# Kernel tuning notes

Measured on AMD Instinct MI355X. Metric: run time of the kernel, lower is better.

Reference implementation:

```python
import jax, jax.numpy as jnp
import numpy as np
from jax import lax

N, D, K, R, T = 200000, 128, 64, 4, 50000
L = 2 * R  # positive + negative relation layers
ITERATIONS = 2


def _l2norm(x, eps=1e-12):
    # torch F.normalize(p=2): x / max(||x||, eps)
    n = jnp.sqrt(jnp.sum(x * x, axis=-1, keepdims=True))
    return x / jnp.maximum(n, eps)


def setup_inputs() -> dict:
    key = jax.random.key(0)
    ks = jax.random.split(key, 8)
    # Unique write targets (a permutation) so the last-write scatter is deterministic;
    # matches input_specs' randint intent (indices uniform in [0, N)).
    perm = jax.random.permutation(ks[0], N)
    subj_idx = perm[:T].astype(jnp.int32)
    obj_idx = perm[T:2 * T].astype(jnp.int32)
    layer_idx = jax.random.randint(ks[1], (T,), 0, L, dtype=jnp.int32)
    memberships = jax.random.randint(ks[2], (N, K), 0, 2, dtype=jnp.int32)
    embedding_m = jax.random.normal(ks[3], (N, D), dtype=jnp.float32)
    # ClassUpdate params: [d+K] -> d
    Wc = jax.random.normal(ks[4], (D + K, D), dtype=jnp.float32) / np.sqrt(D + K)
    bc = jnp.zeros((D,), dtype=jnp.float32)
    # RelationUpdate params, one layer per (relation, polarity): [2d] -> [2d]
    Wr = jax.random.normal(ks[5], (L, 2 * D, 2 * D), dtype=jnp.float32) / np.sqrt(2 * D)
    br = jnp.zeros((L, 2 * D), dtype=jnp.float32)
    return {
        'embedding_m': embedding_m,
        'memberships': memberships,
        'subj_idx': subj_idx,
        'obj_idx': obj_idx,
        'layer_idx': layer_idx,
        'Wc': Wc, 'bc': bc, 'Wr': Wr, 'br': br,
    }


def reference(embedding_m, memberships, subj_idx, obj_idx, layer_idx, Wc, bc, Wr, br):
    mem = memberships.astype(embedding_m.dtype)  # [N, K]
    t_ar = jnp.arange(T)

    def iteration(e, _):
        # --- ClassUpdate: e' = l2norm(tanh([e; m] Wc + bc)) ---
        x = jnp.concatenate([e, mem], axis=1)           # [N, d+K]
        e = _l2norm(jnp.tanh(x @ Wc + bc))              # [N, d]
        # --- RelationUpdates: reads come from the post-class-update snapshot `e`
        pair = jnp.concatenate([e[subj_idx], e[obj_idx]], axis=1)   # [T, 2d]
        # compute through all L relation layers, then select each triple's layer
        out_all = jnp.einsum('tc,lcd->tld', pair, Wr) + br          # [T, L, 2d]
        out = jnp.tanh(out_all[t_ar, layer_idx])                    # [T, 2d]
        new_s = _l2norm(out[:, :D])
        new_o = _l2norm(out[:, D:])
        e_next = e.at[subj_idx].set(new_s).at[obj_idx].set(new_o)
        return e_next, None

    e_final, _ = lax.scan(iteration, embedding_m, None, length=ITERATIONS)
    return e_final
```

## Files before the change

kernel.cpp:

```cpp
#include <hip/hip_runtime.h>
#include <hip/hip_bf16.h>


#define NROWS 200000
#define DD    128
#define KK    64
#define TT    50000
#define LL    8
#define BT    64
#define PADT  50560
#define NPASS 3125

#define NB    100
#define CHB   500
#define PL    8
#define PREPB 268
#define MBB   6250

#define WS_OFFS   0
#define WS_CNT    64
#define WS_BASE   4096
#define WS_BINS   8192
#define WS_WCP    210432
#define WS_WRP    (WS_WCP + 6*8*64*16)
#define WS_MB     (WS_WRP + 8*8*16*64*16)
#define WS_E16    (WS_MB + NROWS*8)
#define WS_NEED   (WS_E16 + (size_t)NROWS*DD*2)

typedef unsigned short u16;
typedef unsigned int   u32;
typedef unsigned long long u64;
typedef unsigned char  u8;
typedef __attribute__((ext_vector_type(8))) short bf16x8;
typedef __attribute__((ext_vector_type(4))) float f32x4;
typedef __attribute__((ext_vector_type(4))) unsigned int u32x4;

#define SWZ(row, byte) ((byte) ^ (((row)&7)<<4))

__device__ __forceinline__ u32 bfbits(float f){
  __hip_bfloat16 h = __float2bfloat16(f);
  return (u32)*reinterpret_cast<unsigned short*>(&h);
}
__device__ __forceinline__ u32 pk(float lo, float hi){
  return bfbits(lo) | (bfbits(hi) << 16);
}
__device__ __forceinline__ float qreduce16(float ss){
  ss += __shfl_xor(ss, 1, 64);
  ss += __shfl_xor(ss, 2, 64);
  ss += __shfl_xor(ss, 4, 64);
  ss += __shfl_xor(ss, 8, 64);
  return ss;
}
__device__ __forceinline__ float fast_tanh(float x){
  float a = fabsf(x);
  float e = __expf(-2.0f*a);
  float t = (1.0f - e) * __builtin_amdgcn_rcpf(1.0f + e);
  return copysignf(t, x);
}
__device__ __forceinline__ float rnorm_scale(float ss){
  return __builtin_amdgcn_rcpf(fmaxf(__builtin_amdgcn_sqrtf(ss), 1e-12f));
}
__device__ __forceinline__ void nt_store_v4(void* p, u32x4 v){
  __builtin_nontemporal_store(v, (u32x4*)p);
}

__global__ __launch_bounds__(256) void k_prep(
    const float* __restrict__ Wc, const float* __restrict__ Wr,
    uint4* __restrict__ wcp, uint4* __restrict__ wrp,
    const int* __restrict__ layer, int* __restrict__ cnt,
    const int* __restrict__ mem, u8* __restrict__ mb8)
{
  if (blockIdx.x >= PREPB + NB){
    int gid = (blockIdx.x - PREPB - NB)*256 + threadIdx.x;
    const int4* s4 = (const int4*)(mem + (size_t)gid*8);
    int4 a = s4[0], b = s4[1];
    u8 byte = (u8)((a.x!=0) | ((a.y!=0)<<1) | ((a.z!=0)<<2) | ((a.w!=0)<<3)
             | ((b.x!=0)<<4) | ((b.y!=0)<<5) | ((b.z!=0)<<6) | ((b.w!=0)<<7));
    __builtin_nontemporal_store(byte, &mb8[gid]);
    return;
  }
  if (blockIdx.x >= PREPB){
    const int bb = blockIdx.x - PREPB, lane = threadIdx.x;
    if (lane >= 64) return;
    const int lim = bb*CHB + CHB;
    int i0 = bb*CHB + lane*PL, i1 = i0 + PL; if (i1 > lim) i1 = lim;
    int c[LL] = {0,0,0,0,0,0,0,0};
    for (int i = i0; i < i1; ++i){
      int l = layer[i];
      #pragma unroll
      for (int k = 0; k < LL; ++k) c[k] += (l == k);
    }
    #pragma unroll
    for (int k = 0; k < LL; ++k){
      int v = c[k];
      v += __shfl_xor(v, 1, 64); v += __shfl_xor(v, 2, 64);
      v += __shfl_xor(v, 4, 64); v += __shfl_xor(v, 8, 64);
      v += __shfl_xor(v, 16, 64); v += __shfl_xor(v, 32, 64);
      if (lane == k) cnt[bb*LL + k] = v;
    }
    return;
  }
  int id = blockIdx.x*blockDim.x + threadIdx.x;
  if (id < 3072){
    int lane = id & 63, nt = (id >> 6) & 7, kt = id >> 9;
    int k0 = kt*32 + (lane>>4)*8, n = nt*16 + (lane&15);
    u32 p[4];
    #pragma unroll
    for (int e2 = 0; e2 < 4; ++e2)
      p[e2] = pk(Wc[(k0 + 2*e2)*DD + n], Wc[(k0 + 2*e2 + 1)*DD + n]);
    wcp[id] = make_uint4(p[0], p[1], p[2], p[3]);
  } else if (id < 3072 + 65536){
    int id2 = id - 3072;
    int lane = id2 & 63, nt = (id2>>6) & 15, kt = (id2>>10) & 7, l = id2 >> 13;
    int k0 = kt*32 + (lane>>4)*8, n = nt*16 + (lane&15);
    const float* w = Wr + (size_t)l*65536;
    u32 p[4];
    #pragma unroll
    for (int e2 = 0; e2 < 4; ++e2)
      p[e2] = pk(w[(k0 + 2*e2)*256 + n], w[(k0 + 2*e2 + 1)*256 + n]);
    wrp[id2] = make_uint4(p[0], p[1], p[2], p[3]);
  }
}

__global__ __launch_bounds__(64) void k_bin2(const int* __restrict__ cnt,
                                             int* __restrict__ offs,
                                             int* __restrict__ gbase,
                                             int* __restrict__ bins)
{
  __shared__ int pre[NB][LL];
  __shared__ int tot[LL], soffs[LL+1];
  const int t = threadIdx.x;
  if (t < LL){
    int acc = 0;
    for (int bb = 0; bb < NB; ++bb){ pre[bb][t] = acc; acc += cnt[bb*LL + t]; }
    tot[t] = acc;
  }
  __syncthreads();
  if (t == 0){
    int acc = 0;
    for (int l = 0; l < LL; ++l){
      soffs[l] = acc; offs[l] = acc;
      acc += ((tot[l] + BT - 1)/BT)*BT;
    }
    soffs[LL] = acc; offs[LL] = acc;
  }
  __syncthreads();
  for (int idx = t; idx < NB*LL; idx += 64){
    int bb = idx >> 3, k = idx & 7;
    gbase[idx] = soffs[k] + pre[bb][k];
  }
  const int k = t >> 3, sub = t & 7;
  const int sz = soffs[k+1] - soffs[k];
  for (int i = tot[k] + sub; i < sz; i += 8) bins[soffs[k] + i] = -1;
}

__global__ __launch_bounds__(64) void k_bin3(const int* __restrict__ layer,
                                             const int* __restrict__ gbase,
                                             int* __restrict__ bins)
{
  const int bb = blockIdx.x, lane = threadIdx.x;
  const int lim = bb*CHB + CHB;
  int i0 = bb*CHB + lane*PL, i1 = i0 + PL; if (i1 > lim) i1 = lim;
  int c[LL] = {0,0,0,0,0,0,0,0};
  for (int i = i0; i < i1; ++i){
    int l = layer[i];
    #pragma unroll
    for (int k = 0; k < LL; ++k) c[k] += (l == k);
  }
  int start[LL];
  #pragma unroll
  for (int k = 0; k < LL; ++k){
    int v = c[k];
    #pragma unroll
    for (int d = 1; d < 64; d <<= 1){
      int u = __shfl_up(v, d, 64);
      if (lane >= d) v += u;
    }
    start[k] = gbase[bb*LL + k] + v - c[k];
  }
  for (int i = i0; i < i1; ++i){
    int l = layer[i];
    #pragma unroll
    for (int k = 0; k < LL; ++k)
      if (l == k) bins[start[k]++] = i;
  }
}

template<bool S16, bool W16, bool WF32>
__global__ __launch_bounds__(256) void k_class(
    const float* __restrict__ srcf, const u16* __restrict__ src16,
    u16* __restrict__ e16, float* __restrict__ dstf,
    const u64* __restrict__ mbits,
    const uint4* __restrict__ wcp, const float* __restrict__ bc)
{
  __shared__ __align__(16) char smem[32768];
  __shared__ float sPart[64][4];
  u16* sA = (u16*)smem;

  const int tid = threadIdx.x;
  const int lane = tid & 63, wid = tid >> 6;
  const int colj = lane & 15, qw = lane >> 4;
  const int rowbase = blockIdx.x * 64;

  int erow[4], ecol[4];
  uint4  eA[4];
  float4 fA[4][2];
  #pragma unroll
  for (int v = 0; v < 4; ++v){
    int f = (v*256 + tid) * 8;
    erow[v] = f >> 7; ecol[v] = f & 127;
    if constexpr (S16){
      eA[v] = *(const uint4*)(src16 + (size_t)(rowbase+erow[v])*DD + ecol[v]);
    } else {
      const float4* s4 = (const float4*)(srcf + (size_t)(rowbase+erow[v])*DD + ecol[v]);
      fA[v][0] = s4[0]; fA[v][1] = s4[1];
    }
  }
  const u64 mv = mbits[rowbase + (tid >> 2)];

  bf16x8 wf[6][2];
  #pragma unroll
  for (int kt = 0; kt < 6; ++kt)
    #pragma unroll
    for (int j = 0; j < 2; ++j)
      wf[kt][j] = *(const bf16x8*)&wcp[(kt*8 + 2*wid + j)*64 + lane];
  const float b0 = bc[(2*wid)*16 + colj];
  const float b1 = bc[(2*wid+1)*16 + colj];

  #pragma unroll
  for (int v = 0; v < 4; ++v){
    uint4 out;
    if constexpr (S16){
      out = eA[v];
    } else {
      float4 a = fA[v][0], b = fA[v][1];
      out = make_uint4(pk(a.x,a.y), pk(a.z,a.w), pk(b.x,b.y), pk(b.z,b.w));
    }
    *(uint4*)((char*)sA + erow[v]*384 + SWZ(erow[v], ecol[v]*2)) = out;
  }
  {
    const int r = tid >> 2, q = tid & 3;
    u32 s = (u32)(mv >> (q*16)) & 0xFFFFu;
    u32 p[8];
    #pragma unroll
    for (int jj = 0; jj < 8; ++jj){
      u32 lo = (s >> (2*jj))     & 1u;
      u32 hi = (s >> (2*jj + 1)) & 1u;
      p[jj] = (lo ? 0x3F80u : 0u) | (hi ? 0x3F800000u : 0u);
    }
    *(uint4*)((char*)sA + r*384 + SWZ(r, 256 + q*32))      = make_uint4(p[0],p[1],p[2],p[3]);
    *(uint4*)((char*)sA + r*384 + SWZ(r, 256 + q*32 + 16)) = make_uint4(p[4],p[5],p[6],p[7]);
  }
  __syncthreads();

  f32x4 acc[4][2];
  #pragma unroll
  for (int m = 0; m < 4; ++m){
    acc[m][0] = (f32x4){0.f,0.f,0.f,0.f};
    acc[m][1] = (f32x4){0.f,0.f,0.f,0.f};
  }
  #pragma unroll
  for (int m = 0; m < 4; ++m){
    int row = m*16 + colj;
    #pragma unroll
    for (int kt = 0; kt < 6; ++kt){
      bf16x8 afr = *(bf16x8*)((char*)sA + row*384 + SWZ(row, kt*64 + qw*16));
      acc[m][0] = __builtin_amdgcn_mfma_f32_16x16x32_bf16(afr, wf[kt][0], acc[m][0], 0,0,0);
      acc[m][1] = __builtin_amdgcn_mfma_f32_16x16x32_bf16(afr, wf[kt][1], acc[m][1], 0,0,0);
    }
  }
  #pragma unroll
  for (int m = 0; m < 4; ++m){
    #pragma unroll
    for (int r = 0; r < 4; ++r){
      float t0 = fast_tanh(acc[m][0][r] + b0);
      float t1 = fast_tanh(acc[m][1][r] + b1);
      acc[m][0][r] = t0; acc[m][1][r] = t1;
      float ss = qreduce16(t0*t0 + t1*t1);
      if (colj == 0) sPart[m*16 + qw*4 + r][wid] = ss;
    }
  }
  __syncthreads();

  #pragma unroll
  for (int m = 0; m < 4; ++m){
    #pragma unroll
    for (int r = 0; r < 4; ++r){
      int tri = m*16 + qw*4 + r;
      f32x4 p = *(f32x4*)sPart[tri];
      float sc = rnorm_scale(p[0] + p[1] + p[2] + p[3]);
      float v0 = acc[m][0][r]*sc, v1 = acc[m][1][r]*sc;
      int c0 = wid*32 + colj;
      if constexpr (W16){
        u16* so = (u16*)smem;
        so[tri*128 + c0]      = (u16)bfbits(v0);
        so[tri*128 + c0 + 16] = (u16)bfbits(v1);
      }
      if constexpr (WF32){
        float* so = (float*)smem;
        so[tri*128 + c0]      = v0;
        so[tri*128 + c0 + 16] = v1;
      }
    }
  }
  __syncthreads();

  if constexpr (W16){
    const u32x4* sp = (const u32x4*)smem;
    u32x4* gp = (u32x4*)(e16 + (size_t)rowbase*DD);
    #pragma unroll
    for (int k = 0; k < 4; ++k)
      nt_store_v4(gp + tid + k*256, sp[tid + k*256]);
  }
  if constexpr (WF32){
    const u32x4* sp = (const u32x4*)smem;
    u32x4* gp = (u32x4*)(dstf + (size_t)rowbase*DD);
    #pragma unroll
    for (int k = 0; k < 8; ++k)
      nt_store_v4(gp + tid + k*256, sp[tid + k*256]);
  }
}

template<bool S16, bool W16, bool WF32>
__global__ __launch_bounds__(256) void k_rel(
    const float* __restrict__ ef32, u16* __restrict__ e16,
    float* __restrict__ dstf,
    const int* __restrict__ subj, const int* __restrict__ obj,
    const uint4* __restrict__ wrp, const float* __restrict__ br,
    const int* __restrict__ offs, const int* __restrict__ bins)
{
  __shared__ __align__(16) char smem[32768];
  __shared__ float sBr[256];
  __shared__ float sPart[BT][4];
  __shared__ int   sS[BT], sO[BT];
  u16* sA = (u16*)smem;

  const int tid  = threadIdx.x;
  const int base = blockIdx.x * BT;
  if (base >= offs[LL]) return;
  int l = 0;
  while (l < LL-1 && base >= offs[l+1]) ++l;

  const int lane = tid & 63, wid = tid >> 6;
  const int colj = lane & 15, qw = lane >> 4;

  const uint4* wb = wrp + (size_t)l*8192 + lane;
  bf16x8 wf[8][4];
  #pragma unroll
  for (int n = 0; n < 4; ++n){
    wf[0][n] = *(const bf16x8*)&wb[(0*16 + wid*4 + n)*64];
    wf[1][n] = *(const bf16x8*)&wb[(1*16 + wid*4 + n)*64];
  }

  sBr[tid] = br[l*256 + tid];

  const int ti = tid >> 2, q = tid & 3;
  int id = bins[base + ti];
  int rs = -1, ro = -1;
  if (id >= 0){ rs = subj[id]; ro = obj[id]; }
  if (q == 0){ sS[ti] = rs; sO[ti] = ro; }
  const int rr = (q < 2) ? rs : ro;
  if constexpr (S16){
    const u16* srcp = e16 + (size_t)rr*DD + (q & 1)*64;
    #pragma unroll
    for (int j = 0; j < 8; ++j){
      uint4 w = (id >= 0) ? ((const uint4*)srcp)[j] : make_uint4(0u,0u,0u,0u);
      *(uint4*)((char*)sA + ti*512 + SWZ(ti, q*128 + j*16)) = w;
    }
  } else {
    const float* srcp = ef32 + (size_t)rr*DD + (q & 1)*64;
    #pragma unroll
    for (int j = 0; j < 8; ++j){
      uint4 w;
      if (id >= 0){
        float4 a = ((const float4*)srcp)[2*j], b = ((const float4*)srcp)[2*j+1];
        w = make_uint4(pk(a.x,a.y), pk(a.z,a.w), pk(b.x,b.y), pk(b.z,b.w));
      } else w = make_uint4(0u,0u,0u,0u);
      *(uint4*)((char*)sA + ti*512 + SWZ(ti, q*128 + j*16)) = w;
    }
  }
  __syncthreads();

  f32x4 acc[4][4];
  #pragma unroll
  for (int m = 0; m < 4; ++m)
    #pragma unroll
    for (int n = 0; n < 4; ++n) acc[m][n] = (f32x4){0.f,0.f,0.f,0.f};

  #pragma unroll
  for (int kt = 0; kt < 8; ++kt){
    if (kt + 2 < 8){
      #pragma unroll
      for (int n = 0; n < 4; ++n)
        wf[kt+2][n] = *(const bf16x8*)&wb[((kt+2)*16 + wid*4 + n)*64];
    }
    #pragma unroll
    for (int m = 0; m < 4; ++m){
      int row = m*16 + colj;
      bf16x8 afr = *(bf16x8*)((char*)sA + row*512 + SWZ(row, kt*64 + qw*16));
      #pragma unroll
      for (int n = 0; n < 4; ++n)
        acc[m][n] = __builtin_amdgcn_mfma_f32_16x16x32_bf16(afr, wf[kt][n], acc[m][n], 0,0,0);
    }
  }

  #pragma unroll
  for (int m = 0; m < 4; ++m){
    #pragma unroll
    for (int n = 0; n < 4; ++n){
      float b = sBr[(wid*4 + n)*16 + colj];
      #pragma unroll
      for (int r = 0; r < 4; ++r)
        acc[m][n][r] = fast_tanh(acc[m][n][r] + b);
    }
    #pragma unroll
    for (int r = 0; r < 4; ++r){
      float ss = acc[m][0][r]*acc[m][0][r] + acc[m][1][r]*acc[m][1][r]
               + acc[m][2][r]*acc[m][2][r] + acc[m][3][r]*acc[m][3][r];
      ss = qreduce16(ss);
      if (colj == 0) sPart[m*16 + qw*4 + r][wid] = ss;
    }
  }
  __syncthreads();

  const int h = wid >> 1;
  if constexpr (W16){
    #pragma unroll
    for (int m = 0; m < 4; ++m){
      #pragma unroll
      for (int r = 0; r < 4; ++r){
        int tri = m*16 + qw*4 + r;
        float ss = sPart[tri][2*h] + sPart[tri][2*h + 1];
        float sc = rnorm_scale(ss);
        #pragma unroll
        for (int n = 0; n < 4; ++n){
          int col = (wid*4 + n)*16 + colj;
          float v = acc[m][n][r]*sc;
          *(u16*)((char*)smem + tri*512 + ((col*2) ^ ((tri&7)<<4))) = (u16)bfbits(v);
        }
      }
    }
    __syncthreads();
    #pragma unroll
    for (int k = 0; k < 8; ++k){
      int c = tid + k*256;
      int tri = c >> 5, hh = (c >> 4) & 1, sub = c & 15;
      int row = hh ? sO[tri] : sS[tri];
      if (row >= 0){
        u32x4 v = *(const u32x4*)((char*)smem + ((c*16) ^ ((tri&7)<<4)));
        nt_store_v4((u32x4*)(e16 + (size_t)row*DD) + sub, v);
      }
    }
  }
  if constexpr (WF32){
    #pragma unroll
    for (int m = 0; m < 4; ++m){
      #pragma unroll
      for (int r = 0; r < 4; ++r){
        int tri = m*16 + qw*4 + r;
        int row = h ? sO[tri] : sS[tri];
        if (row < 0) continue;
        float ss = sPart[tri][2*h] + sPart[tri][2*h + 1];
        float sc = rnorm_scale(ss);
        #pragma unroll
        for (int n = 0; n < 4; ++n){
          int cc = (wid*4 + n)*16 + colj - h*DD;
          __builtin_nontemporal_store(acc[m][n][r]*sc, &dstf[(size_t)row*DD + cc]);
        }
      }
    }
  }
}

extern "C" void kernel_launch(void* const* d_in, const int* in_sizes, int n_in,
                              void* d_out, int out_size, void* d_ws, size_t ws_size,
                              hipStream_t stream) {
  (void)in_sizes; (void)n_in; (void)out_size;
  const float* emb  = (const float*)d_in[0];
  const int*   mem  = (const int*)  d_in[1];
  const int*   subj = (const int*)  d_in[2];
  const int*   obj  = (const int*)  d_in[3];
  const int*   lay  = (const int*)  d_in[4];
  const float* Wc   = (const float*)d_in[5];
  const float* bc   = (const float*)d_in[6];
  const float* Wr   = (const float*)d_in[7];
  const float* br   = (const float*)d_in[8];

  float* e   = (float*)d_out;
  char*  wsb = (char*)d_ws;
  int*   offs  = (int*)(wsb + WS_OFFS);
  int*   cnt   = (int*)(wsb + WS_CNT);
  int*   gbase = (int*)(wsb + WS_BASE);
  int*   bins  = (int*)(wsb + WS_BINS);
  uint4* wcp   = (uint4*)(wsb + WS_WCP);
  uint4* wrp   = (uint4*)(wsb + WS_WRP);
  u64*   mbits = (u64*)(wsb + WS_MB);
  u8*    mb8   = (u8*)(wsb + WS_MB);
  u16*   e16   = (u16*)(wsb + WS_E16);

  k_prep<<<PREPB + NB + MBB, 256, 0, stream>>>(Wc, Wr, wcp, wrp, lay, cnt, mem, mb8);
  k_bin2<<<1, 64, 0, stream>>>(cnt, offs, gbase, bins);
  k_bin3<<<NB, 64, 0, stream>>>(lay, gbase, bins);

  if (ws_size >= WS_NEED){
    k_class<false,true,false><<<NPASS, 256, 0, stream>>>(
        emb, nullptr, e16, nullptr, mbits, wcp, bc);
    k_rel<true,true,false><<<PADT/BT, 256, 0, stream>>>(
        nullptr, e16, nullptr, subj, obj, wrp, br, offs, bins);
    k_class<true,false,true><<<NPASS, 256, 0, stream>>>(
        nullptr, e16, nullptr, e, mbits, wcp, bc);
    k_rel<false,false,true><<<PADT/BT, 256, 0, stream>>>(
        e, nullptr, e, subj, obj, wrp, br, offs, bins);
  } else {
    k_class<false,false,true><<<NPASS, 256, 0, stream>>>(
        emb, nullptr, nullptr, e, mbits, wcp, bc);
    k_rel<false,false,true><<<PADT/BT, 256, 0, stream>>>(
        e, nullptr, e, subj, obj, wrp, br, offs, bins);
    k_class<false,false,true><<<NPASS, 256, 0, stream>>>(
        e, nullptr, nullptr, e, mbits, wcp, bc);
    k_rel<false,false,true><<<PADT/BT, 256, 0, stream>>>(
        e, nullptr, e, subj, obj, wrp, br, offs, bins);
  }
}
```

Baseline: 172.0 us.

## Split class-update work across 8 waves and write fp32 output directly

After: 174.6 us. About the same (+1.5%).

```diff
diff --git a/kernel.cpp b/kernel.cpp
--- a/kernel.cpp
+++ b/kernel.cpp
@@ -187,14 +187,15 @@
 }
 
 template<bool S16, bool W16, bool WF32>
-__global__ __launch_bounds__(256) void k_class(
+__global__ __launch_bounds__(512) void k_class(
     const float* __restrict__ srcf, const u16* __restrict__ src16,
     u16* __restrict__ e16, float* __restrict__ dstf,
     const u64* __restrict__ mbits,
     const uint4* __restrict__ wcp, const float* __restrict__ bc)
 {
-  __shared__ __align__(16) char smem[32768];
-  __shared__ float sPart[64][4];
+  __shared__ __align__(16) char smem[24576];
+  __shared__ float sPart[64][9];
+  __shared__ float sScale[64];
   u16* sA = (u16*)smem;
 
   const int tid = threadIdx.x;
@@ -202,43 +203,41 @@
   const int colj = lane & 15, qw = lane >> 4;
   const int rowbase = blockIdx.x * 64;
 
-  int erow[4], ecol[4];
-  uint4  eA[4];
-  float4 fA[4][2];
-  #pragma unroll
-  for (int v = 0; v < 4; ++v){
-    int f = (v*256 + tid) * 8;
-    erow[v] = f >> 7; ecol[v] = f & 127;
+  int crow[2], ccc[2];
+  uint4  eA[2];
+  float4 fA[2][2];
+  #pragma unroll
+  for (int v = 0; v < 2; ++v){
+    int c = tid + v*512;
+    crow[v] = c >> 4; ccc[v] = c & 15;
     if constexpr (S16){
-      eA[v] = *(const uint4*)(src16 + (size_t)(rowbase+erow[v])*DD + ecol[v]);
+      eA[v] = *(const uint4*)(src16 + (size_t)(rowbase+crow[v])*DD + ccc[v]*8);
     } else {
-      const float4* s4 = (const float4*)(srcf + (size_t)(rowbase+erow[v])*DD + ecol[v]);
+      const float4* s4 = (const float4*)(srcf + (size_t)(rowbase+crow[v])*DD + ccc[v]*8);
       fA[v][0] = s4[0]; fA[v][1] = s4[1];
     }
   }
-  const u64 mv = mbits[rowbase + (tid >> 2)];
-
-  bf16x8 wf[6][2];
+  u64 mv = 0;
+  if (tid < 256) mv = mbits[rowbase + (tid >> 2)];
+
+  bf16x8 wf[6];
   #pragma unroll
   for (int kt = 0; kt < 6; ++kt)
-    #pragma unroll
-    for (int j = 0; j < 2; ++j)
-      wf[kt][j] = *(const bf16x8*)&wcp[(kt*8 + 2*wid + j)*64 + lane];
-  const float b0 = bc[(2*wid)*16 + colj];
-  const float b1 = bc[(2*wid+1)*16 + colj];
-
-  #pragma unroll
-  for (int v = 0; v < 4; ++v){
+    wf[kt] = *(const bf16x8*)&wcp[(kt*8 + wid)*64 + lane];
+  const float b = bc[wid*16 + colj];
+
+  #pragma unroll
+  for (int v = 0; v < 2; ++v){
     uint4 out;
     if constexpr (S16){
       out = eA[v];
     } else {
-      float4 a = fA[v][0], b = fA[v][1];
-      out = make_uint4(pk(a.x,a.y), pk(a.z,a.w), pk(b.x,b.y), pk(b.z,b.w));
-    }
-    *(uint4*)((char*)sA + erow[v]*384 + SWZ(erow[v], ecol[v]*2)) = out;
-  }
-  {
+      float4 a = fA[v][0], bb2 = fA[v][1];
+      out = make_uint4(pk(a.x,a.y), pk(a.z,a.w), pk(bb2.x,bb2.y), pk(bb2.z,bb2.w));
+    }
+    *(uint4*)((char*)sA + crow[v]*384 + SWZ(crow[v], ccc[v]*16)) = out;
+  }
+  if (tid < 256){
     const int r = tid >> 2, q = tid & 3;
     u32 s = (u32)(mv >> (q*16)) & 0xFFFFu;
     u32 p[8];
@@ -253,71 +252,62 @@
   }
   __syncthreads();
 
-  f32x4 acc[4][2];
-  #pragma unroll
-  for (int m = 0; m < 4; ++m){
-    acc[m][0] = (f32x4){0.f,0.f,0.f,0.f};
-    acc[m][1] = (f32x4){0.f,0.f,0.f,0.f};
-  }
+  f32x4 acc[4];
+  #pragma unroll
+  for (int m = 0; m < 4; ++m) acc[m] = (f32x4){0.f,0.f,0.f,0.f};
   #pragma unroll
   for (int m = 0; m < 4; ++m){
     int row = m*16 + colj;
     #pragma unroll
     for (int kt = 0; kt < 6; ++kt){
       bf16x8 afr = *(bf16x8*)((char*)sA + row*384 + SWZ(row, kt*64 + qw*16));
-      acc[m][0] = __builtin_amdgcn_mfma_f32_16x16x32_bf16(afr, wf[kt][0], acc[m][0], 0,0,0);
-      acc[m][1] = __builtin_amdgcn_mfma_f32_16x16x32_bf16(afr, wf[kt][1], acc[m][1], 0,0,0);
+      acc[m] = __builtin_amdgcn_mfma_f32_16x16x32_bf16(afr, wf[kt], acc[m], 0,0,0);
     }
   }
   #pragma unroll
   for (int m = 0; m < 4; ++m){
     #pragma unroll
     for (int r = 0; r < 4; ++r){
-      float t0 = fast_tanh(acc[m][0][r] + b0);
-      float t1 = fast_tanh(acc[m][1][r] + b1);
-      acc[m][0][r] = t0; acc[m][1][r] = t1;
-      float ss = qreduce16(t0*t0 + t1*t1);
+      float t = fast_tanh(acc[m][r] + b);
+      acc[m][r] = t;
+      float ss = qreduce16(t*t);
       if (colj == 0) sPart[m*16 + qw*4 + r][wid] = ss;
     }
   }
   __syncthreads();
-
-  #pragma unroll
-  for (int m = 0; m < 4; ++m){
-    #pragma unroll
-    for (int r = 0; r < 4; ++r){
-      int tri = m*16 + qw*4 + r;
-      f32x4 p = *(f32x4*)sPart[tri];
-      float sc = rnorm_scale(p[0] + p[1] + p[2] + p[3]);
-      float v0 = acc[m][0][r]*sc, v1 = acc[m][1][r]*sc;
-      int c0 = wid*32 + colj;
-      if constexpr (W16){
-        u16* so = (u16*)smem;
-        so[tri*128 + c0]      = (u16)bfbits(v0);
-        so[tri*128 + c0 + 16] = (u16)bfbits(v1);
+  if (tid < 64){
+    float s = 0.f;
+    #pragma unroll
+    for (int i = 0; i < 8; ++i) s += sPart[tid][i];
+    sScale[tid] = rnorm_scale(s);
+  }
+  __syncthreads();
+
+  if constexpr (W16){
+    u16* so = (u16*)smem;
+    #pragma unroll
+    for (int m = 0; m < 4; ++m){
+      #pragma unroll
+      for (int r = 0; r < 4; ++r){
+        int row = m*16 + qw*4 + r;
+        so[row*128 + wid*16 + colj] = (u16)bfbits(acc[m][r]*sScale[row]);
       }
-      if constexpr (WF32){
-        float* so = (float*)smem;
-        so[tri*128 + c0]      = v0;
-        so[tri*128 + c0 + 16] = v1;
-      }
-    }
-  }
-  __syncthreads();
-
-  if constexpr (W16){
+    }
+    __syncthreads();
     const u32x4* sp = (const u32x4*)smem;
     u32x4* gp = (u32x4*)(e16 + (size_t)rowbase*DD);
-    #pragma unroll
-    for (int k = 0; k < 4; ++k)
-      nt_store_v4(gp + tid + k*256, sp[tid + k*256]);
+    nt_store_v4(gp + tid,       sp[tid]);
+    nt_store_v4(gp + tid + 512, sp[tid + 512]);
   }
   if constexpr (WF32){
-    const u32x4* sp = (const u32x4*)smem;
-    u32x4* gp = (u32x4*)(dstf + (size_t)rowbase*DD);
-    #pragma unroll
-    for (int k = 0; k < 8; ++k)
-      nt_store_v4(gp + tid + k*256, sp[tid + k*256]);
+    #pragma unroll
+    for (int m = 0; m < 4; ++m){
+      #pragma unroll
+      for (int r = 0; r < 4; ++r){
+        int row = m*16 + qw*4 + r;
+        dstf[(size_t)(rowbase+row)*DD + wid*16 + colj] = acc[m][r]*sScale[row];
+      }
+    }
   }
 }
 
@@ -465,7 +455,7 @@
         #pragma unroll
         for (int n = 0; n < 4; ++n){
           int cc = (wid*4 + n)*16 + colj - h*DD;
-          __builtin_nontemporal_store(acc[m][n][r]*sc, &dstf[(size_t)row*DD + cc]);
+          dstf[(size_t)row*DD + cc] = acc[m][n][r]*sc;
         }
       }
     }
@@ -503,20 +493,20 @@
   k_bin3<<<NB, 64, 0, stream>>>(lay, gbase, bins);
 
   if (ws_size >= WS_NEED){
-    k_class<false,true,false><<<NPASS, 256, 0, stream>>>(
+    k_class<false,true,false><<<NPASS, 512, 0, stream>>>(
         emb, nullptr, e16, nullptr, mbits, wcp, bc);
     k_rel<true,true,false><<<PADT/BT, 256, 0, stream>>>(
         nullptr, e16, nullptr, subj, obj, wrp, br, offs, bins);
-    k_class<true,false,true><<<NPASS, 256, 0, stream>>>(
+    k_class<true,false,true><<<NPASS, 512, 0, stream>>>(
         nullptr, e16, nullptr, e, mbits, wcp, bc);
     k_rel<false,false,true><<<PADT/BT, 256, 0, stream>>>(
         e, nullptr, e, subj, obj, wrp, br, offs, bins);
   } else {
-    k_class<false,false,true><<<NPASS, 256, 0, stream>>>(
+    k_class<false,false,true><<<NPASS, 512, 0, stream>>>(
         emb, nullptr, nullptr, e, mbits, wcp, bc);
     k_rel<false,false,true><<<PADT/BT, 256, 0, stream>>>(
         e, nullptr, e, subj, obj, wrp, br, offs, bins);
-    k_class<false,false,true><<<NPASS, 256, 0, stream>>>(
+    k_class<false,false,true><<<NPASS, 512, 0, stream>>>(
         e, nullptr, nullptr, e, mbits, wcp, bc);
     k_rel<false,false,true><<<PADT/BT, 256, 0, stream>>>(
         e, nullptr, e, subj, obj, wrp, br, offs, bins);
```

## Fuse class and relation phases into one persistent cooperative kernel with grid syncs

Applied to the files above, without the earlier changes.

Result: slower. 437.6 us (+154.4%).

```diff
diff --git a/kernel.cpp b/kernel.cpp
--- a/kernel.cpp
+++ b/kernel.cpp
@@ -1,5 +1,8 @@
 #include <hip/hip_runtime.h>
 #include <hip/hip_bf16.h>
+#include <hip/hip_cooperative_groups.h>
+
+namespace cg = cooperative_groups;
 
 
 #define NROWS 200000
@@ -9,6 +12,7 @@
 #define LL    8
 #define BT    64
 #define PADT  50560
+#define NGRP  (PADT/BT)
 #define NPASS 3125
 
 #define NB    100
@@ -27,6 +31,13 @@
 #define WS_E16    (WS_MB + NROWS*8)
 #define WS_NEED   (WS_E16 + (size_t)NROWS*DD*2)
 
+#define SM_BYTES  35328
+#define SM_SA     0
+#define SM_BR     32768
+#define SM_PART   33792
+#define SM_SS     34816
+#define SM_SO     35072
+
 typedef unsigned short u16;
 typedef unsigned int   u32;
 typedef unsigned long long u64;
@@ -186,37 +197,19 @@
   }
 }
 
-template<bool S16, bool W16, bool WF32>
-__global__ __launch_bounds__(256) void k_class(
+template<bool S16, bool W16>
+__device__ void class_phase(char* smem,
     const float* __restrict__ srcf, const u16* __restrict__ src16,
-    u16* __restrict__ e16, float* __restrict__ dstf,
+    u16* __restrict__ e16o, float* __restrict__ dstf,
     const u64* __restrict__ mbits,
     const uint4* __restrict__ wcp, const float* __restrict__ bc)
 {
-  __shared__ __align__(16) char smem[32768];
-  __shared__ float sPart[64][4];
   u16* sA = (u16*)smem;
+  float (*sPart)[4] = (float(*)[4])(smem + SM_PART);
 
   const int tid = threadIdx.x;
   const int lane = tid & 63, wid = tid >> 6;
   const int colj = lane & 15, qw = lane >> 4;
-  const int rowbase = blockIdx.x * 64;
-
-  int erow[4], ecol[4];
-  uint4  eA[4];
-  float4 fA[4][2];
-  #pragma unroll
-  for (int v = 0; v < 4; ++v){
-    int f = (v*256 + tid) * 8;
-    erow[v] = f >> 7; ecol[v] = f & 127;
-    if constexpr (S16){
-      eA[v] = *(const uint4*)(src16 + (size_t)(rowbase+erow[v])*DD + ecol[v]);
-    } else {
-      const float4* s4 = (const float4*)(srcf + (size_t)(rowbase+erow[v])*DD + ecol[v]);
-      fA[v][0] = s4[0]; fA[v][1] = s4[1];
-    }
-  }
-  const u64 mv = mbits[rowbase + (tid >> 2)];
 
   bf16x8 wf[6][2];
   #pragma unroll
@@ -227,249 +220,310 @@
   const float b0 = bc[(2*wid)*16 + colj];
   const float b1 = bc[(2*wid+1)*16 + colj];
 
-  #pragma unroll
-  for (int v = 0; v < 4; ++v){
-    uint4 out;
-    if constexpr (S16){
-      out = eA[v];
+  for (int t = blockIdx.x; t < NPASS; t += gridDim.x){
+    const int rowbase = t * 64;
+    int erow[4], ecol[4];
+    uint4  eA[4];
+    float4 fA[4][2];
+    #pragma unroll
+    for (int v = 0; v < 4; ++v){
+      int f = (v*256 + tid) * 8;
+      erow[v] = f >> 7; ecol[v] = f & 127;
+      if constexpr (S16){
+        eA[v] = *(const uint4*)(src16 + (size_t)(rowbase+erow[v])*DD + ecol[v]);
+      } else {
+        const float4* s4 = (const float4*)(srcf + (size_t)(rowbase+erow[v])*DD + ecol[v]);
+        fA[v][0] = s4[0]; fA[v][1] = s4[1];
+      }
+    }
+    const u64 mv = mbits[rowbase + (tid >> 2)];
+    __syncthreads();
+    #pragma unroll
+    for (int v = 0; v < 4; ++v){
+      uint4 out;
+      if constexpr (S16){
+        out = eA[v];
+      } else {
+        float4 a = fA[v][0], b = fA[v][1];
+        out = make_uint4(pk(a.x,a.y), pk(a.z,a.w), pk(b.x,b.y), pk(b.z,b.w));
+      }
+      *(uint4*)((char*)sA + erow[v]*384 + SWZ(erow[v], ecol[v]*2)) = out;
+    }
+    {
+      const int r = tid >> 2, q = tid & 3;
+      u32 s = (u32)(mv >> (q*16)) & 0xFFFFu;
+      u32 p[8];
+      #pragma unroll
+      for (int jj = 0; jj < 8; ++jj){
+        u32 lo = (s >> (2*jj))     & 1u;
+        u32 hi = (s >> (2*jj + 1)) & 1u;
+        p[jj] = (lo ? 0x3F80u : 0u) | (hi ? 0x3F800000u : 0u);
+      }
+      *(uint4*)((char*)sA + r*384 + SWZ(r, 256 + q*32))      = make_uint4(p[0],p[1],p[2],p[3]);
+      *(uint4*)((char*)sA + r*384 + SWZ(r, 256 + q*32 + 16)) = make_uint4(p[4],p[5],p[6],p[7]);
+    }
+    __syncthreads();
+
+    f32x4 acc[4][2];
+    #pragma unroll
+    for (int m = 0; m < 4; ++m){
+      acc[m][0] = (f32x4){0.f,0.f,0.f,0.f};
+      acc[m][1] = (f32x4){0.f,0.f,0.f,0.f};
+    }
+    #pragma unroll
+    for (int m = 0; m < 4; ++m){
+      int row = m*16 + colj;
+      #pragma unroll
+      for (int kt = 0; kt < 6; ++kt){
+        bf16x8 afr = *(bf16x8*)((char*)sA + row*384 + SWZ(row, kt*64 + qw*16));
+        acc[m][0] = __builtin_amdgcn_mfma_f32_16x16x32_bf16(afr, wf[kt][0], acc[m][0], 0,0,0);
+        acc[m][1] = __builtin_amdgcn_mfma_f32_16x16x32_bf16(afr, wf[kt][1], acc[m][1], 0,0,0);
+      }
+    }
+    #pragma unroll
+    for (int m = 0; m < 4; ++m){
+      #pragma unroll
+      for (int r = 0; r < 4; ++r){
+        float t0 = fast_tanh(acc[m][0][r] + b0);
+        float t1 = fast_tanh(acc[m][1][r] + b1);
+        acc[m][0][r] = t0; acc[m][1][r] = t1;
+        float ss = qreduce16(t0*t0 + t1*t1);
+        if (colj == 0) sPart[m*16 + qw*4 + r][wid] = ss;
+      }
+    }
+    __syncthreads();
+
+    if constexpr (W16){
+      u16* so = (u16*)smem;
+      #pragma unroll
+      for (int m = 0; m < 4; ++m){
+        #pragma unroll
+        for (int r = 0; r < 4; ++r){
+          int tri = m*16 + qw*4 + r;
+          f32x4 p = *(f32x4*)sPart[tri];
+          float sc = rnorm_scale(p[0] + p[1] + p[2] + p[3]);
+          int c0 = wid*32 + colj;
+          so[tri*128 + c0]      = (u16)bfbits(acc[m][0][r]*sc);
+          so[tri*128 + c0 + 16] = (u16)bfbits(acc[m][1][r]*sc);
+        }
+      }
+      __syncthreads();
+      const u32x4* sp = (const u32x4*)smem;
+      u32x4* gp = (u32x4*)(e16o + (size_t)rowbase*DD);
+      #pragma unroll
+      for (int k = 0; k < 4; ++k)
+        nt_store_v4(gp + tid + k*256, sp[tid + k*256]);
     } else {
-      float4 a = fA[v][0], b = fA[v][1];
-      out = make_uint4(pk(a.x,a.y), pk(a.z,a.w), pk(b.x,b.y), pk(b.z,b.w));
-    }
-    *(uint4*)((char*)sA + erow[v]*384 + SWZ(erow[v], ecol[v]*2)) = out;
-  }
-  {
-    const int r = tid >> 2, q = tid & 3;
-    u32 s = (u32)(mv >> (q*16)) & 0xFFFFu;
-    u32 p[8];
-    #pragma unroll
-    for (int jj = 0; jj < 8; ++jj){
-      u32 lo = (s >> (2*jj))     & 1u;
-      u32 hi = (s >> (2*jj + 1)) & 1u;
-      p[jj] = (lo ? 0x3F80u : 0u) | (hi ? 0x3F800000u : 0u);
-    }
-    *(uint4*)((char*)sA + r*384 + SWZ(r, 256 + q*32))      = make_uint4(p[0],p[1],p[2],p[3]);
-    *(uint4*)((char*)sA + r*384 + SWZ(r, 256 + q*32 + 16)) = make_uint4(p[4],p[5],p[6],p[7]);
-  }
-  __syncthreads();
-
-  f32x4 acc[4][2];
-  #pragma unroll
-  for (int m = 0; m < 4; ++m){
-    acc[m][0] = (f32x4){0.f,0.f,0.f,0.f};
-    acc[m][1] = (f32x4){0.f,0.f,0.f,0.f};
-  }
-  #pragma unroll
-  for (int m = 0; m < 4; ++m){
-    int row = m*16 + colj;
-    #pragma unroll
-    for (int kt = 0; kt < 6; ++kt){
-      bf16x8 afr = *(bf16x8*)((char*)sA + row*384 + SWZ(row, kt*64 + qw*16));
-      acc[m][0] = __builtin_amdgcn_mfma_f32_16x16x32_bf16(afr, wf[kt][0], acc[m][0], 0,0,0);
-      acc[m][1] = __builtin_amdgcn_mfma_f32_16x16x32_bf16(afr, wf[kt][1], acc[m][1], 0,0,0);
-    }
-  }
-  #pragma unroll
-  for (int m = 0; m < 4; ++m){
-    #pragma unroll
-    for (int r = 0; r < 4; ++r){
-      float t0 = fast_tanh(acc[m][0][r] + b0);
-      float t1 = fast_tanh(acc[m][1][r] + b1);
-      acc[m][0][r] = t0; acc[m][1][r] = t1;
-      float ss = qreduce16(t0*t0 + t1*t1);
-      if (colj == 0) sPart[m*16 + qw*4 + r][wid] = ss;
-    }
-  }
-  __syncthreads();
-
-  #pragma unroll
-  for (int m = 0; m < 4; ++m){
-    #pragma unroll
-    for (int r = 0; r < 4; ++r){
-      int tri = m*16 + qw*4 + r;
-      f32x4 p = *(f32x4*)sPart[tri];
-      float sc = rnorm_scale(p[0] + p[1] + p[2] + p[3]);
-      float v0 = acc[m][0][r]*sc, v1 = acc[m][1][r]*sc;
-      int c0 = wid*32 + colj;
-      if constexpr (W16){
-        u16* so = (u16*)smem;
-        so[tri*128 + c0]      = (u16)bfbits(v0);
-        so[tri*128 + c0 + 16] = (u16)bfbits(v1);
-      }
-      if constexpr (WF32){
-        float* so = (float*)smem;
-        so[tri*128 + c0]      = v0;
-        so[tri*128 + c0 + 16] = v1;
-      }
-    }
-  }
-  __syncthreads();
-
-  if constexpr (W16){
-    const u32x4* sp = (const u32x4*)smem;
-    u32x4* gp = (u32x4*)(e16 + (size_t)rowbase*DD);
-    #pragma unroll
-    for (int k = 0; k < 4; ++k)
-      nt_store_v4(gp + tid + k*256, sp[tid + k*256]);
-  }
-  if constexpr (WF32){
-    const u32x4* sp = (const u32x4*)smem;
-    u32x4* gp = (u32x4*)(dstf + (size_t)rowbase*DD);
-    #pragma unroll
-    for (int k = 0; k < 8; ++k)
-      nt_store_v4(gp + tid + k*256, sp[tid + k*256]);
-  }
-}
-
-template<bool S16, bool W16, bool WF32>
-__global__ __launch_bounds__(256) void k_rel(
+      #pragma unroll
+      for (int m = 0; m < 4; ++m){
+        #pragma unroll
+        for (int r = 0; r < 4; ++r){
+          int row = m*16 + qw*4 + r;
+          f32x4 p = *(f32x4*)sPart[row];
+          float sc = rnorm_scale(p[0] + p[1] + p[2] + p[3]);
+          size_t g = (size_t)(rowbase+row)*DD;
+          dstf[g + (2*wid)*16 + colj]   = acc[m][0][r]*sc;
+          dstf[g + (2*wid+1)*16 + colj] = acc[m][1][r]*sc;
+        }
+      }
+    }
+  }
+}
+
+template<bool S16, bool W16>
+__device__ void rel_phase(char* smem,
     const float* __restrict__ ef32, u16* __restrict__ e16,
     float* __restrict__ dstf,
     const int* __restrict__ subj, const int* __restrict__ obj,
     const uint4* __restrict__ wrp, const float* __restrict__ br,
     const int* __restrict__ offs, const int* __restrict__ bins)
 {
-  __shared__ __align__(16) char smem[32768];
-  __shared__ float sBr[256];
-  __shared__ float sPart[BT][4];
-  __shared__ int   sS[BT], sO[BT];
-  u16* sA = (u16*)smem;
+  u16*   sA    = (u16*)smem;
+  float* sBr   = (float*)(smem + SM_BR);
+  float (*sPart)[4] = (float(*)[4])(smem + SM_PART);
+  int*   sS    = (int*)(smem + SM_SS);
+  int*   sO    = (int*)(smem + SM_SO);
 
   const int tid  = threadIdx.x;
-  const int base = blockIdx.x * BT;
-  if (base >= offs[LL]) return;
-  int l = 0;
-  while (l < LL-1 && base >= offs[l+1]) ++l;
-
   const int lane = tid & 63, wid = tid >> 6;
   const int colj = lane & 15, qw = lane >> 4;
-
-  const uint4* wb = wrp + (size_t)l*8192 + lane;
-  bf16x8 wf[8][4];
-  #pragma unroll
-  for (int n = 0; n < 4; ++n){
-    wf[0][n] = *(const bf16x8*)&wb[(0*16 + wid*4 + n)*64];
-    wf[1][n] = *(const bf16x8*)&wb[(1*16 + wid*4 + n)*64];
-  }
-
-  sBr[tid] = br[l*256 + tid];
-
-  const int ti = tid >> 2, q = tid & 3;
-  int id = bins[base + ti];
-  int rs = -1, ro = -1;
-  if (id >= 0){ rs = subj[id]; ro = obj[id]; }
-  if (q == 0){ sS[ti] = rs; sO[ti] = ro; }
-  const int rr = (q < 2) ? rs : ro;
-  if constexpr (S16){
-    const u16* srcp = e16 + (size_t)rr*DD + (q & 1)*64;
-    #pragma unroll
-    for (int j = 0; j < 8; ++j){
-      uint4 w = (id >= 0) ? ((const uint4*)srcp)[j] : make_uint4(0u,0u,0u,0u);
-      *(uint4*)((char*)sA + ti*512 + SWZ(ti, q*128 + j*16)) = w;
-    }
-  } else {
-    const float* srcp = ef32 + (size_t)rr*DD + (q & 1)*64;
-    #pragma unroll
-    for (int j = 0; j < 8; ++j){
-      uint4 w;
-      if (id >= 0){
-        float4 a = ((const float4*)srcp)[2*j], b = ((const float4*)srcp)[2*j+1];
-        w = make_uint4(pk(a.x,a.y), pk(a.z,a.w), pk(b.x,b.y), pk(b.z,b.w));
-      } else w = make_uint4(0u,0u,0u,0u);
-      *(uint4*)((char*)sA + ti*512 + SWZ(ti, q*128 + j*16)) = w;
-    }
-  }
-  __syncthreads();
-
-  f32x4 acc[4][4];
-  #pragma unroll
-  for (int m = 0; m < 4; ++m)
-    #pragma unroll
-    for (int n = 0; n < 4; ++n) acc[m][n] = (f32x4){0.f,0.f,0.f,0.f};
-
-  #pragma unroll
-  for (int kt = 0; kt < 8; ++kt){
-    if (kt + 2 < 8){
-      #pragma unroll
-      for (int n = 0; n < 4; ++n)
-        wf[kt+2][n] = *(const bf16x8*)&wb[((kt+2)*16 + wid*4 + n)*64];
-    }
+  const int total = offs[LL];
+
+  for (int g = blockIdx.x; g < NGRP; g += gridDim.x){
+    const int base = g * BT;
+    __syncthreads();
+    if (base >= total) continue;
+    int l = 0;
+    while (l < LL-1 && base >= offs[l+1]) ++l;
+
+    const uint4* wb = wrp + (size_t)l*8192 + lane;
+    bf16x8 wf[8][4];
+    #pragma unroll
+    for (int n = 0; n < 4; ++n){
+      wf[0][n] = *(const bf16x8*)&wb[(0*16 + wid*4 + n)*64];
+      wf[1][n] = *(const bf16x8*)&wb[(1*16 + wid*4 + n)*64];
+    }
+    sBr[tid] = br[l*256 + tid];
+
+    const int ti = tid >> 2, q = tid & 3;
+    int id = bins[base + ti];
+    int rs = -1, ro = -1;
+    if (id >= 0){ rs = subj[id]; ro = obj[id]; }
+    if (q == 0){ sS[ti] = rs; sO[ti] = ro; }
+    const int rr = (q < 2) ? rs : ro;
+    if constexpr (S16){
+      const u16* srcp = e16 + (size_t)rr*DD + (q & 1)*64;
+      #pragma unroll
+      for (int j = 0; j < 8; ++j){
+        uint4 w = (id >= 0) ? ((const uint4*)srcp)[j] : make_uint4(0u,0u,0u,0u);
+        *(uint4*)((char*)sA + ti*512 + SWZ(ti, q*128 + j*16)) = w;
+      }
+    } else {
+      const float* srcp = ef32 + (size_t)rr*DD + (q & 1)*64;
+      #pragma unroll
+      for (int j = 0; j < 8; ++j){
+        uint4 w;
+        if (id >= 0){
+          float4 a = ((const float4*)srcp)[2*j], b = ((const float4*)srcp)[2*j+1];
+          w = make_uint4(pk(a.x,a.y), pk(a.z,a.w), pk(b.x,b.y), pk(b.z,b.w));
+        } else w = make_uint4(0u,0u,0u,0u);
+        *(uint4*)((char*)sA + ti*512 + SWZ(ti, q*128 + j*16)) = w;
+      }
+    }
+    __syncthreads();
+
+    f32x4 acc[4][4];
+    #pragma unroll
+    for (int m = 0; m < 4; ++m)
+      #pragma unroll
+      for (int n = 0; n < 4; ++n) acc[m][n] = (f32x4){0.f,0.f,0.f,0.f};
+
+    #pragma unroll
+    for (int kt = 0; kt < 8; ++kt){
+      if (kt + 2 < 8){
+        #pragma unroll
+        for (int n = 0; n < 4; ++n)
+          wf[kt+2][n] = *(const bf16x8*)&wb[((kt+2)*16 + wid*4 + n)*64];
+      }
+      #pragma unroll
+      for (int m = 0; m < 4; ++m){
+        int row = m*16 + colj;
+        bf16x8 afr = *(bf16x8*)((char*)sA + row*512 + SWZ(row, kt*64 + qw*16));
+        #pragma unroll
+        for (int n = 0; n < 4; ++n)
+          acc[m][n] = __builtin_amdgcn_mfma_f32_16x16x32_bf16(afr, wf[kt][n], acc[m][n], 0,0,0);
+      }
+    }
+
     #pragma unroll
     for (int m = 0; m < 4; ++m){
-      int row = m*16 + colj;
-      bf16x8 afr = *(bf16x8*)((char*)sA + row*512 + SWZ(row, kt*64 + qw*16));
-      #pragma unroll
-      for (int n = 0; n < 4; ++n)
-        acc[m][n] = __builtin_amdgcn_mfma_f32_16x16x32_bf16(afr, wf[kt][n], acc[m][n], 0,0,0);
-    }
-  }
-
-  #pragma unroll
-  for (int m = 0; m < 4; ++m){
-    #pragma unroll
-    for (int n = 0; n < 4; ++n){
-      float b = sBr[(wid*4 + n)*16 + colj];
-      #pragma unroll
-      for (int r = 0; r < 4; ++r)
-        acc[m][n][r] = fast_tanh(acc[m][n][r] + b);
-    }
-    #pragma unroll
-    for (int r = 0; r < 4; ++r){
-      float ss = acc[m][0][r]*acc[m][0][r] + acc[m][1][r]*acc[m][1][r]
-               + acc[m][2][r]*acc[m][2][r] + acc[m][3][r]*acc[m][3][r];
-      ss = qreduce16(ss);
-      if (colj == 0) sPart[m*16 + qw*4 + r][wid] = ss;
-    }
-  }
-  __syncthreads();
-
-  const int h = wid >> 1;
-  if constexpr (W16){
-    #pragma unroll
-    for (int m = 0; m < 4; ++m){
+      #pragma unroll
+      for (int n = 0; n < 4; ++n){
+        float b = sBr[(wid*4 + n)*16 + colj];
+        #pragma unroll
+        for (int r = 0; r < 4; ++r)
+          acc[m][n][r] = fast_tanh(acc[m][n][r] + b);
+      }
       #pragma unroll
       for (int r = 0; r < 4; ++r){
-        int tri = m*16 + qw*4 + r;
-        float ss = sPart[tri][2*h] + sPart[tri][2*h + 1];
-        float sc = rnorm_scale(ss);
-        #pragma unroll
-        for (int n = 0; n < 4; ++n){
-          int col = (wid*4 + n)*16 + colj;
-          float v = acc[m][n][r]*sc;
-          *(u16*)((char*)smem + tri*512 + ((col*2) ^ ((tri&7)<<4))) = (u16)bfbits(v);
+        float ss = acc[m][0][r]*acc[m][0][r] + acc[m][1][r]*acc[m][1][r]
+                 + acc[m][2][r]*acc[m][2][r] + acc[m][3][r]*acc[m][3][r];
+        ss = qreduce16(ss);
+        if (colj == 0) sPart[m*16 + qw*4 + r][wid] = ss;
+      }
+    }
+    __syncthreads();
+
+    const int h = wid >> 1;
+    if constexpr (W16){
+      #pragma unroll
+      for (int m = 0; m < 4; ++m){
+        #pragma unroll
+        for (int r = 0; r < 4; ++r){
+          int tri = m*16 + qw*4 + r;
+          float ss = sPart[tri][2*h] + sPart[tri][2*h + 1];
+          float sc = rnorm_scale(ss);
+          #pragma unroll
+          for (int n = 0; n < 4; ++n){
+            int col = (wid*4 + n)*16 + colj;
+            float v = acc[m][n][r]*sc;
+            *(u16*)((char*)smem + tri*512 + ((col*2) ^ ((tri&7)<<4))) = (u16)bfbits(v);
+          }
         }
       }
-    }
-    __syncthreads();
-    #pragma unroll
-    for (int k = 0; k < 8; ++k){
-      int c = tid + k*256;
-      int tri = c >> 5, hh = (c >> 4) & 1, sub = c & 15;
-      int row = hh ? sO[tri] : sS[tri];
-      if (row >= 0){
-        u32x4 v = *(const u32x4*)((char*)smem + ((c*16) ^ ((tri&7)<<4)));
-        nt_store_v4((u32x4*)(e16 + (size_t)row*DD) + sub, v);
-      }
-    }
-  }
-  if constexpr (WF32){
-    #pragma unroll
-    for (int m = 0; m < 4; ++m){
-      #pragma unroll
-      for (int r = 0; r < 4; ++r){
-        int tri = m*16 + qw*4 + r;
-        int row = h ? sO[tri] : sS[tri];
-        if (row < 0) continue;
-        float ss = sPart[tri][2*h] + sPart[tri][2*h + 1];
-        float sc = rnorm_scale(ss);
-        #pragma unroll
-        for (int n = 0; n < 4; ++n){
-          int cc = (wid*4 + n)*16 + colj - h*DD;
-          __builtin_nontemporal_store(acc[m][n][r]*sc, &dstf[(size_t)row*DD + cc]);
+      __syncthreads();
+      #pragma unroll
+      for (int k = 0; k < 8; ++k){
+        int c = tid + k*256;
+        int tri = c >> 5, hh = (c >> 4) & 1, sub = c & 15;
+        int row = hh ? sO[tri] : sS[tri];
+        if (row >= 0){
+          u32x4 v = *(const u32x4*)((char*)smem + ((c*16) ^ ((tri&7)<<4)));
+          nt_store_v4((u32x4*)(e16 + (size_t)row*DD) + sub, v);
         }
       }
-    }
-  }
+    } else {
+      #pragma unroll
+      for (int m = 0; m < 4; ++m){
+        #pragma unroll
+        for (int r = 0; r < 4; ++r){
+          int tri = m*16 + qw*4 + r;
+          int row = h ? sO[tri] : sS[tri];
+          if (row < 0) continue;
+          float ss = sPart[tri][2*h] + sPart[tri][2*h + 1];
+          float sc = rnorm_scale(ss);
+          #pragma unroll
+          for (int n = 0; n < 4; ++n){
+            int cc = (wid*4 + n)*16 + colj - h*DD;
+            dstf[(size_t)row*DD + cc] = acc[m][n][r]*sc;
+          }
+        }
+      }
+    }
+  }
+}
+
+__global__ __launch_bounds__(256) void k_main(
+    const float* __restrict__ emb, u16* __restrict__ e16,
+    float* __restrict__ eout, const u64* __restrict__ mbits,
+    const uint4* __restrict__ wcp, const float* __restrict__ bc,
+    const int* __restrict__ subj, const int* __restrict__ obj,
+    const uint4* __restrict__ wrp, const float* __restrict__ br,
+    const int* __restrict__ offs, const int* __restrict__ bins)
+{
+  __shared__ __align__(16) char smem[SM_BYTES];
+  cg::grid_group grid = cg::this_grid();
+
+  class_phase<false,true>(smem, emb, nullptr, e16, nullptr, mbits, wcp, bc);
+  grid.sync();
+  rel_phase<true,true>(smem, nullptr, e16, nullptr, subj, obj, wrp, br, offs, bins);
+  grid.sync();
+  class_phase<true,false>(smem, nullptr, e16, nullptr, eout, mbits, wcp, bc);
+  grid.sync();
+  rel_phase<false,false>(smem, eout, nullptr, eout, subj, obj, wrp, br, offs, bins);
+}
+
+template<bool S16, bool W16>
+__global__ __launch_bounds__(256) void k_class_sa(
+    const float* __restrict__ srcf, const u16* __restrict__ src16,
+    u16* __restrict__ e16o, float* __restrict__ dstf,
+    const u64* __restrict__ mbits,
+    const uint4* __restrict__ wcp, const float* __restrict__ bc)
+{
+  __shared__ __align__(16) char smem[SM_BYTES];
+  class_phase<S16,W16>(smem, srcf, src16, e16o, dstf, mbits, wcp, bc);
+}
+
+template<bool S16, bool W16>
+__global__ __launch_bounds__(256) void k_rel_sa(
+    const float* __restrict__ ef32, u16* __restrict__ e16,
+    float* __restrict__ dstf,
+    const int* __restrict__ subj, const int* __restrict__ obj,
+    const uint4* __restrict__ wrp, const float* __restrict__ br,
+    const int* __restrict__ offs, const int* __restrict__ bins)
+{
+  __shared__ __align__(16) char smem[SM_BYTES];
+  rel_phase<S16,W16>(smem, ef32, e16, dstf, subj, obj, wrp, br, offs, bins);
 }
 
 extern "C" void kernel_launch(void* const* d_in, const int* in_sizes, int n_in,
@@ -488,37 +542,52 @@
 
   float* e   = (float*)d_out;
   char*  wsb = (char*)d_ws;
-  int*   offs  = (int*)(wsb + WS_OFFS);
+  const int*   offs  = (const int*)(wsb + WS_OFFS);
   int*   cnt   = (int*)(wsb + WS_CNT);
   int*   gbase = (int*)(wsb + WS_BASE);
-  int*   bins  = (int*)(wsb + WS_BINS);
-  uint4* wcp   = (uint4*)(wsb + WS_WCP);
-  uint4* wrp   = (uint4*)(wsb + WS_WRP);
-  u64*   mbits = (u64*)(wsb + WS_MB);
+  const int*   bins  = (const int*)(wsb + WS_BINS);
+  const uint4* wcp   = (const uint4*)(wsb + WS_WCP);
+  const uint4* wrp   = (const uint4*)(wsb + WS_WRP);
+  const u64*   mbits = (const u64*)(wsb + WS_MB);
   u8*    mb8   = (u8*)(wsb + WS_MB);
   u16*   e16   = (u16*)(wsb + WS_E16);
 
-  k_prep<<<PREPB + NB + MBB, 256, 0, stream>>>(Wc, Wr, wcp, wrp, lay, cnt, mem, mb8);
-  k_bin2<<<1, 64, 0, stream>>>(cnt, offs, gbase, bins);
-  k_bin3<<<NB, 64, 0, stream>>>(lay, gbase, bins);
-
-  if (ws_size >= WS_NEED){
-    k_class<false,true,false><<<NPASS, 256, 0, stream>>>(
+  k_prep<<<PREPB + NB + MBB, 256, 0, stream>>>(
+      Wc, Wr, (uint4*)wcp, (uint4*)wrp, lay, cnt, mem, mb8);
+  k_bin2<<<1, 64, 0, stream>>>(cnt, (int*)offs, gbase, (int*)bins);
+  k_bin3<<<NB, 64, 0, stream>>>(lay, gbase, (int*)bins);
+
+  const bool full = (ws_size >= WS_NEED);
+  int coop = 0, dev = 0, occ = 0;
+  hipGetDevice(&dev);
+  hipDeviceGetAttribute(&coop, hipDeviceAttributeCooperativeLaunch, dev);
+  hipOccupancyMaxActiveBlocksPerMultiprocessor(&occ, k_main, 256, 0);
+
+  if (full && coop && occ >= 1){
+    int grid = occ * 256; if (grid > 1024) grid = 1024;
+    void* args[12];
+    args[0] = (void*)&emb;  args[1] = (void*)&e16;  args[2] = (void*)&e;
+    args[3] = (void*)&mbits; args[4] = (void*)&wcp; args[5] = (void*)&bc;
+    args[6] = (void*)&subj; args[7] = (void*)&obj;  args[8] = (void*)&wrp;
+    args[9] = (void*)&br;   args[10] = (void*)&offs; args[11] = (void*)&bins;
+    hipLaunchCooperativeKernel(k_main, dim3(grid), dim3(256), args, 0, stream);
+  } else if (full){
+    k_class_sa<false,true><<<NPASS, 256, 0, stream>>>(
         emb, nullptr, e16, nullptr, mbits, wcp, bc);
-    k_rel<true,true,false><<<PADT/BT, 256, 0, stream>>>(
+    k_rel_sa<true,true><<<NGRP, 256, 0, stream>>>(
         nullptr, e16, nullptr, subj, obj, wrp, br, offs, bins);
-    k_class<true,false,true><<<NPASS, 256, 0, stream>>>(
+    k_class_sa<true,false><<<NPASS, 256, 0, stream>>>(
         nullptr, e16, nullptr, e, mbits, wcp, bc);
-    k_rel<false,false,true><<<PADT/BT, 256, 0, stream>>>(
+    k_rel_sa<false,false><<<NGRP, 256, 0, stream>>>(
         e, nullptr, e, subj, obj, wrp, br, offs, bins);
   } else {
-    k_class<false,false,true><<<NPASS, 256, 0, stream>>>(
+    k_class_sa<false,false><<<NPASS, 256, 0, stream>>>(
         emb, nullptr, nullptr, e, mbits, wcp, bc);
-    k_rel<false,false,true><<<PADT/BT, 256, 0, stream>>>(
+    k_rel_sa<false,false><<<NGRP, 256, 0, stream>>>(
         e, nullptr, e, subj, obj, wrp, br, offs, bins);
-    k_class<false,false,true><<<NPASS, 256, 0, stream>>>(
+    k_class_sa<false,false><<<NPASS, 256, 0, stream>>>(
         e, nullptr, nullptr, e, mbits, wcp, bc);
-    k_rel<false,false,true><<<PADT/BT, 256, 0, stream>>>(
+    k_rel_sa<false,false><<<NGRP, 256, 0, stream>>>(
         e, nullptr, e, subj, obj, wrp, br, offs, bins);
   }
 }
```
